# Performance work log

Measured on AMD Instinct MI355X. Metric: run time of the kernel, lower is better.

## Reference

```python
import jax, jax.numpy as jnp
import numpy as np

S = 4096          # seq_len (longformer-large-4096)
H = 1024          # hidden_size
FF = 3072         # ffnn_size (hardcoded)
G = 100           # number of gold mentions
MAX_SPAN = 30     # max_span_length
TOP_LAMBDA = 0.2
LN_EPS = 1e-5
MASK_VAL = 10000.0


def setup_inputs() -> dict:
    key = jax.random.key(0)
    ks = jax.random.split(key, 16)
    sc = 0.02
    sequence_output = jax.random.normal(ks[0], (1, S, H), jnp.float32)
    attention_mask = jnp.ones((1, S), jnp.int32)
    # valid gold spans: 1 <= start <= end < start + MAX_SPAN (so torch's >0 filter keeps all)
    gs = jax.random.randint(ks[1], (G,), 1, S - MAX_SPAN)
    gl = jax.random.randint(ks[2], (G,), 0, MAX_SPAN)
    gold_mentions = jnp.stack([gs, gs + gl], axis=1).astype(jnp.int32)  # [G, 2]
    inp = {
        'sequence_output': sequence_output,
        'attention_mask': attention_mask,
        'gold_mentions': gold_mentions,
        # start_mention_mlp
        'W_sm': jax.random.normal(ks[3], (H, FF), jnp.float32) * sc,
        'b_sm': jnp.zeros((FF,), jnp.float32),
        'g_sm': jnp.ones((FF,), jnp.float32),
        'beta_sm': jnp.zeros((FF,), jnp.float32),
        # end_mention_mlp
        'W_em': jax.random.normal(ks[4], (H, FF), jnp.float32) * sc,
        'b_em': jnp.zeros((FF,), jnp.float32),
        'g_em': jnp.ones((FF,), jnp.float32),
        'beta_em': jnp.zeros((FF,), jnp.float32),
        # classifiers
        'w_start': jax.random.normal(ks[5], (FF,), jnp.float32) * sc,
        'b_start': jnp.zeros((), jnp.float32),
        'w_end': jax.random.normal(ks[6], (FF,), jnp.float32) * sc,
        'b_end': jnp.zeros((), jnp.float32),
        'W_s2e': jax.random.normal(ks[7], (FF, FF), jnp.float32) * sc,
        'b_s2e': jnp.zeros((FF,), jnp.float32),
    }
    return inp


def _fcl(x, W, b, g, beta):
    # dense -> gelu (exact) -> layernorm (dropout is identity in eval)
    h = jax.nn.gelu(x @ W + b, approximate=False)
    mu = jnp.mean(h, axis=-1, keepdims=True)
    var = jnp.mean(jnp.square(h - mu), axis=-1, keepdims=True)
    return (h - mu) * jax.lax.rsqrt(var + LN_EPS) * g + beta


def _forward(sequence_output, attention_mask, gold_mentions,
             W_sm, b_sm, g_sm, beta_sm, W_em, b_em, g_em, beta_em,
             w_start, b_start, w_end, b_end, W_s2e, b_s2e):
    start_reps = _fcl(sequence_output, W_sm, b_sm, g_sm, beta_sm)  # [1,S,FF]
    end_reps = _fcl(sequence_output, W_em, b_em, g_em, beta_em)    # [1,S,FF]

    start_logits = jnp.einsum('bsf,f->bs', start_reps, w_start) + b_start  # [1,S]
    end_logits = jnp.einsum('bsf,f->bs', end_reps, w_end) + b_end          # [1,S]
    temp = start_reps @ W_s2e + b_s2e                                      # [1,S,FF]
    joint = jnp.einsum('bsf,btf->bst', temp, end_reps)                     # [1,S,S]
    mention_logits = joint + start_logits[:, :, None] + end_logits[:, None, :]

    # span mask: start <= end < start + MAX_SPAN (triu(0) then tril(MAX_SPAN-1))
    i = jnp.arange(S)
    mention_mask = ((i[:, None] <= i[None, :]) & (i[None, :] < i[:, None] + MAX_SPAN)
                    ).astype(jnp.float32)[None]  # [1,S,S]
    mention_logits = jnp.clip(mention_logits + (1.0 - mention_mask) * (-MASK_VAL),
                              -MASK_VAL, MASK_VAL)

    # top-k pruning; attention_mask is full so k is static: int(S * 0.2)
    max_k = int(S * TOP_LAMBDA)  # 819
    _, topk_1d = jax.lax.top_k(mention_logits.reshape(1, -1), max_k)  # [1,max_k]
    sorted_idx = jnp.sort(topk_1d, axis=-1)
    topk_start_ids = sorted_idx // S
    topk_end_ids = sorted_idx % S
    span_mask = jnp.ones((1, max_k), jnp.float32)

    # losses
    probs = jax.nn.sigmoid(mention_logits)  # [1,S,S]
    gstart = gold_mentions[:, 0]
    gend = gold_mentions[:, 1]
    gold_probs = probs[0, gstart, gend]
    # torch BCE clamps log at -100
    cost_gold = -jnp.mean(jnp.maximum(jnp.log(gold_probs), -100.0))
    junk = probs.at[0, gstart, gend].set(0.0)
    log1mp = jnp.maximum(jnp.log(1.0 - junk), -100.0)
    cost_junk = -jnp.sum(jnp.where(mention_mask == 1.0, log1mp, 0.0)) / jnp.sum(mention_mask)
    cost_is_mention = (cost_gold + cost_junk)[None]  # [1]

    return topk_start_ids, topk_end_ids, span_mask, sequence_output, cost_is_mention


def reference(sequence_output, attention_mask, gold_mentions,
              W_sm, b_sm, g_sm, beta_sm, W_em, b_em, g_em, beta_em,
              w_start, b_start, w_end, b_end, W_s2e, b_s2e):
    return _forward(sequence_output, attention_mask, gold_mentions,
                    W_sm, b_sm, g_sm, beta_sm, W_em, b_em, g_em, beta_em,
                    w_start, b_start, w_end, b_end, W_s2e, b_s2e)
```

## Files before the change

kernel.cpp:

```cpp
#include <hip/hip_runtime.h>
#include <math.h>

#define S 4096
#define H 1024
#define FF 3072
#define G 100
#define MAXSPAN 30
#define MAXK 819
#define NBAND (S * MAXSPAN)
#define BAND_COUNT 122445.0

#define O_START 0
#define O_END   819
#define O_MASK  1638
#define O_SEQ   2457
#define O_COST  (2457 + S * H)

typedef __bf16 bf16x8 __attribute__((ext_vector_type(8)));
typedef float f32x4 __attribute__((ext_vector_type(4)));
typedef float f32x16 __attribute__((ext_vector_type(16)));


__device__ __forceinline__ float block_reduce_256(float x, volatile float* red) {
  #pragma unroll
  for (int off = 32; off > 0; off >>= 1) x += __shfl_down(x, off, 64);
  int wid = threadIdx.x >> 6;
  int lane = threadIdx.x & 63;
  __syncthreads();
  if (lane == 0) red[wid] = x;
  __syncthreads();
  return red[0] + red[1] + red[2] + red[3];
}

__device__ __forceinline__ unsigned f2key(float f) {
  unsigned b = __float_as_uint(f);
  return (b & 0x80000000u) ? ~b : (b | 0x80000000u);
}

__device__ __forceinline__ unsigned short bf16_rne(float x) {
  unsigned u = __float_as_uint(x);
  unsigned r = ((u >> 16) & 1u) + 0x7FFFu;
  return (unsigned short)((u + r) >> 16);
}

__device__ __forceinline__ void split2(float x, unsigned short& h, unsigned short& l) {
  h = bf16_rne(x);
  float hf = __uint_as_float(((unsigned)h) << 16);
  l = bf16_rne(x - hf);
}

__device__ __forceinline__ void gld16(const void* g, void* l) {
  __builtin_amdgcn_global_load_lds(
      (const __attribute__((address_space(1))) unsigned int*)g,
      (__attribute__((address_space(3))) unsigned int*)l, 16, 0, 0);
}


__global__ __launch_bounds__(256) void pack_a_kernel(const float* __restrict__ A,
                                                     unsigned short* __restrict__ hi,
                                                     unsigned short* __restrict__ lo,
                                                     int K) {
  __shared__ float tile[32][33];
  const int t = threadIdx.x;
  const int tx = t & 31, ty8 = t >> 5;
  const int k0 = blockIdx.x * 32, r0 = blockIdx.y * 32;
  #pragma unroll
  for (int r = ty8; r < 32; r += 8)
    tile[r][tx] = A[(size_t)(r0 + r) * K + k0 + tx];
  __syncthreads();
  if (t < 128) {
    const int kql = t >> 5;
    const int rl = t & 31;
    unsigned short h8[8], l8[8];
    #pragma unroll
    for (int s = 0; s < 8; s++) split2(tile[rl][kql * 8 + s], h8[s], l8[s]);
    const size_t panel = (size_t)(r0 >> 7);
    const int rloc = (r0 & 127) + rl;
    const size_t off = panel * (size_t)(128 * K) + (size_t)(k0 / 8 + kql) * 1024 + (size_t)rloc * 8;
    *(uint4*)(hi + off) = *(const uint4*)h8;
    *(uint4*)(lo + off) = *(const uint4*)l8;
  }
}

__global__ __launch_bounds__(256) void pack_ln_a_kernel(const float* __restrict__ A,
                                                        const float* __restrict__ mu,
                                                        const float* __restrict__ rstd,
                                                        const float* __restrict__ g,
                                                        const float* __restrict__ beta,
                                                        unsigned short* __restrict__ hi,
                                                        unsigned short* __restrict__ lo,
                                                        int K) {
  __shared__ float tile[32][33];
  const int t = threadIdx.x;
  const int tx = t & 31, ty8 = t >> 5;
  const int k0 = blockIdx.x * 32, r0 = blockIdx.y * 32;
  #pragma unroll
  for (int r = ty8; r < 32; r += 8)
    tile[r][tx] = A[(size_t)(r0 + r) * K + k0 + tx];
  __syncthreads();
  if (t < 128) {
    const int kql = t >> 5;
    const int rl = t & 31;
    const int row = r0 + rl;
    const float m = mu[row], rs = rstd[row];
    float4 g0 = *(const float4*)(g + k0 + kql * 8);
    float4 g1 = *(const float4*)(g + k0 + kql * 8 + 4);
    float4 b0 = *(const float4*)(beta + k0 + kql * 8);
    float4 b1 = *(const float4*)(beta + k0 + kql * 8 + 4);
    float gv[8] = {g0.x, g0.y, g0.z, g0.w, g1.x, g1.y, g1.z, g1.w};
    float bv[8] = {b0.x, b0.y, b0.z, b0.w, b1.x, b1.y, b1.z, b1.w};
    unsigned short h8[8], l8[8];
    #pragma unroll
    for (int s = 0; s < 8; s++) {
      float v = (tile[rl][kql * 8 + s] - m) * rs * gv[s] + bv[s];
      split2(v, h8[s], l8[s]);
    }
    const size_t panel = (size_t)(r0 >> 7);
    const int rloc = (r0 & 127) + rl;
    const size_t off = panel * (size_t)(128 * K) + (size_t)(k0 / 8 + kql) * 1024 + (size_t)rloc * 8;
    *(uint4*)(hi + off) = *(const uint4*)h8;
    *(uint4*)(lo + off) = *(const uint4*)l8;
  }
}

__global__ __launch_bounds__(256) void pack_bt_kernel(const float* __restrict__ W,
                                                      unsigned short* __restrict__ hi,
                                                      unsigned short* __restrict__ lo,
                                                      int K, int N) {
  __shared__ float tile[32][33];
  const int t = threadIdx.x;
  const int tx = t & 31, ty8 = t >> 5;
  const int k0 = blockIdx.x * 32, n0 = blockIdx.y * 32;
  #pragma unroll
  for (int r = ty8; r < 32; r += 8)
    tile[r][tx] = W[(size_t)(k0 + r) * N + n0 + tx];
  __syncthreads();
  if (t < 128) {
    const int kql = t >> 5;
    const int nl = t & 31;
    unsigned short h8[8], l8[8];
    #pragma unroll
    for (int s = 0; s < 8; s++) split2(tile[kql * 8 + s][nl], h8[s], l8[s]);
    const size_t panel = (size_t)(n0 >> 7);
    const int nloc = (n0 & 127) + nl;
    const size_t off = panel * (size_t)(128 * K) + (size_t)(k0 / 8 + kql) * 1024 + (size_t)nloc * 8;
    *(uint4*)(hi + off) = *(const uint4*)h8;
    *(uint4*)(lo + off) = *(const uint4*)l8;
  }
}


template <int EPI>
__global__ __launch_bounds__(256) void gemm_mfma_kernel(const unsigned short* __restrict__ Ahi,
                                                        const unsigned short* __restrict__ Alo,
                                                        const unsigned short* __restrict__ Bhi,
                                                        const unsigned short* __restrict__ Blo,
                                                        const float* __restrict__ bias,
                                                        float* __restrict__ C,
                                                        int M, int N, int K) {
  __shared__ __align__(16) char smem[32768];
  const int tid = threadIdx.x;
  const int lane = tid & 63;
  const int wid = __builtin_amdgcn_readfirstlane(tid >> 6);
  const int wm = wid >> 1, wn = wid & 1;
  const int bm = blockIdx.y * 128, bn = blockIdx.x * 128;

  const size_t panAb = (size_t)blockIdx.y * (size_t)(128 * K) * 2;
  const size_t panBb = (size_t)blockIdx.x * (size_t)(128 * K) * 2;
  const char* cAh = (const char*)Ahi + panAb;
  const char* cAl = (const char*)Alo + panAb;
  const char* cBh = (const char*)Bhi + panBb;
  const char* cBl = (const char*)Blo + panBb;
  const int lb = lane * 16;
  const int ldsq = wid * 2048;

  const int khalf = lane >> 5;
  const int r31 = lane & 31;
  const int abase = khalf * 2048 + (wm * 64 + r31) * 16;
  const int bbase = khalf * 2048 + (wn * 64 + r31) * 16;

  f32x16 acc[2][2];
  #pragma unroll
  for (int a = 0; a < 2; a++)
    #pragma unroll
    for (int b = 0; b < 2; b++)
      #pragma unroll
      for (int r = 0; r < 16; r++) acc[a][b][r] = 0.0f;

  for (int k0 = 0; k0 < K; k0 += 32) {
    const size_t qb = (size_t)((k0 >> 3) + wid) * 2048 + lb;
    __syncthreads();
    gld16(cAh + qb,        smem +     0 + ldsq);
    gld16(cAh + qb + 1024, smem +     0 + ldsq + 1024);
    gld16(cAl + qb,        smem +  8192 + ldsq);
    gld16(cAl + qb + 1024, smem +  8192 + ldsq + 1024);
    gld16(cBh + qb,        smem + 16384 + ldsq);
    gld16(cBh + qb + 1024, smem + 16384 + ldsq + 1024);
    gld16(cBl + qb,        smem + 24576 + ldsq);
    gld16(cBl + qb + 1024, smem + 24576 + ldsq + 1024);
    __syncthreads();

    bf16x8 ah[2][2], al[2][2], bh[2][2], bl[2][2];
    #pragma unroll
    for (int ks = 0; ks < 2; ks++) {
      #pragma unroll
      for (int mt = 0; mt < 2; mt++) {
        ah[ks][mt] = *(const bf16x8*)(smem +     0 + ks * 4096 + abase + mt * 512);
        al[ks][mt] = *(const bf16x8*)(smem +  8192 + ks * 4096 + abase + mt * 512);
      }
      #pragma unroll
      for (int nt = 0; nt < 2; nt++) {
        bh[ks][nt] = *(const bf16x8*)(smem + 16384 + ks * 4096 + bbase + nt * 512);
        bl[ks][nt] = *(const bf16x8*)(smem + 24576 + ks * 4096 + bbase + nt * 512);
      }
    }
    #pragma unroll
    for (int ks = 0; ks < 2; ks++)
      #pragma unroll
      for (int mt = 0; mt < 2; mt++)
        #pragma unroll
        for (int nt = 0; nt < 2; nt++) {
          acc[mt][nt] = __builtin_amdgcn_mfma_f32_32x32x16_bf16(ah[ks][mt], bh[ks][nt], acc[mt][nt], 0, 0, 0);
          acc[mt][nt] = __builtin_amdgcn_mfma_f32_32x32x16_bf16(al[ks][mt], bh[ks][nt], acc[mt][nt], 0, 0, 0);
          acc[mt][nt] = __builtin_amdgcn_mfma_f32_32x32x16_bf16(ah[ks][mt], bl[ks][nt], acc[mt][nt], 0, 0, 0);
        }
  }

  #pragma unroll
  for (int mt = 0; mt < 2; mt++) {
    #pragma unroll
    for (int nt = 0; nt < 2; nt++) {
      const int colg = bn + wn * 64 + nt * 32 + r31;
      const float bb = bias[colg];
      #pragma unroll
      for (int reg = 0; reg < 16; reg++) {
        const int rowl = (reg & 3) + 8 * (reg >> 2) + 4 * khalf;
        const int rowg = bm + wm * 64 + mt * 32 + rowl;
        float v = acc[mt][nt][reg] + bb;
        if (EPI == 1) v = 0.5f * v * (1.0f + erff(v * 0.70710678118654752f));
        C[(size_t)rowg * N + colg] = v;
      }
    }
  }
}


template <int WRITEBACK>
__global__ __launch_bounds__(256) void ln_dot_kernel(float* __restrict__ Hb,
                                                     const float* __restrict__ g,
                                                     const float* __restrict__ beta,
                                                     const float* __restrict__ w,
                                                     const float* __restrict__ bsc,
                                                     float* __restrict__ logits,
                                                     float* __restrict__ mu_out,
                                                     float* __restrict__ rstd_out) {
  __shared__ float red[4];
  const int row = blockIdx.x, tid = threadIdx.x;
  float* h = Hb + (size_t)row * FF;

  float4 v[3];
  float s = 0.0f;
  #pragma unroll
  for (int t = 0; t < 3; t++) {
    v[t] = *(const float4*)(h + tid * 4 + t * 1024);
    s += v[t].x + v[t].y + v[t].z + v[t].w;
  }
  float mu = block_reduce_256(s, red) * (1.0f / (float)FF);

  float s2 = 0.0f;
  #pragma unroll
  for (int t = 0; t < 3; t++) {
    float dx = v[t].x - mu, dy = v[t].y - mu, dz = v[t].z - mu, dw = v[t].w - mu;
    s2 += dx * dx + dy * dy + dz * dz + dw * dw;
  }
  float var = block_reduce_256(s2, red) * (1.0f / (float)FF);
  float rstd = rsqrtf(var + 1e-5f);

  float dot = 0.0f;
  #pragma unroll
  for (int t = 0; t < 3; t++) {
    int idx = tid * 4 + t * 1024;
    float4 gv = *(const float4*)(g + idx);
    float4 bv = *(const float4*)(beta + idx);
    float4 wv = *(const float4*)(w + idx);
    float4 r;
    r.x = (v[t].x - mu) * rstd * gv.x + bv.x;
    r.y = (v[t].y - mu) * rstd * gv.y + bv.y;
    r.z = (v[t].z - mu) * rstd * gv.z + bv.z;
    r.w = (v[t].w - mu) * rstd * gv.w + bv.w;
    if (WRITEBACK) *(float4*)(h + idx) = r;
    dot += r.x * wv.x + r.y * wv.y + r.z * wv.z + r.w * wv.w;
  }
  float dt = block_reduce_256(dot, red);
  if (tid == 0) {
    logits[row] = dt + bsc[0];
    if (!WRITEBACK) { mu_out[row] = mu; rstd_out[row] = rstd; }
  }
}


__global__ __launch_bounds__(256) void band_joint_kernel(const float* __restrict__ T,
                                                         const float* __restrict__ E,
                                                         const float* __restrict__ sl,
                                                         const float* __restrict__ el,
                                                         float* __restrict__ band) {
  __shared__ float Elds[45][260];
  const int t = threadIdx.x;
  const int i0 = blockIdx.x * 16;
  const int r_l = t >> 4, c = t & 15;

  float accd[MAXSPAN];
  #pragma unroll
  for (int d = 0; d < MAXSPAN; d++) accd[d] = 0.0f;

  for (int k0 = 0; k0 < FF; k0 += 256) {
    const float* trow = T + (size_t)(i0 + r_l) * FF + k0 + c * 16;
    float4 tv0 = *(const float4*)(trow + 0);
    float4 tv1 = *(const float4*)(trow + 4);
    float4 tv2 = *(const float4*)(trow + 8);
    float4 tv3 = *(const float4*)(trow + 12);
    __syncthreads();
    for (int rr = t >> 6; rr < 45; rr += 4) {
      int gr = i0 + rr;
      int cc = (t & 63) * 4;
      float4 ev = {0.f, 0.f, 0.f, 0.f};
      if (gr < S) ev = *(const float4*)(E + (size_t)gr * FF + k0 + cc);
      *(float4*)&Elds[rr][cc] = ev;
    }
    __syncthreads();
    #pragma unroll
    for (int d = 0; d < MAXSPAN; d++) {
      const float* er = &Elds[r_l + d][c * 16];
      float4 e0 = *(const float4*)(er + 0);
      float4 e1 = *(const float4*)(er + 4);
      float4 e2 = *(const float4*)(er + 8);
      float4 e3 = *(const float4*)(er + 12);
      accd[d] += tv0.x * e0.x + tv0.y * e0.y + tv0.z * e0.z + tv0.w * e0.w
               + tv1.x * e1.x + tv1.y * e1.y + tv1.z * e1.z + tv1.w * e1.w
               + tv2.x * e2.x + tv2.y * e2.y + tv2.z * e2.z + tv2.w * e2.w
               + tv3.x * e3.x + tv3.y * e3.y + tv3.z * e3.z + tv3.w * e3.w;
    }
  }

  const int i = i0 + r_l;
  const float my_sl = sl[i];
  #pragma unroll
  for (int d = 0; d < MAXSPAN; d++) {
    float v = accd[d];
    v += __shfl_down(v, 8, 16);
    v += __shfl_down(v, 4, 16);
    v += __shfl_down(v, 2, 16);
    v += __shfl_down(v, 1, 16);
    if (c == 0) {
      int j = i + d;
      if (j < S) {
        float vv = v + my_sl + el[j];
        vv = fminf(fmaxf(vv, -10000.0f), 10000.0f);
        band[i * MAXSPAN + d] = vv;
      } else {
        band[i * MAXSPAN + d] = -1e30f;
      }
    }
  }
}


__global__ void mark_gold_kernel(const int* __restrict__ gold, char* __restrict__ mark) {
  int t = threadIdx.x;
  if (t < G) {
    int gs = gold[2 * t], ge = gold[2 * t + 1];
    mark[gs * MAXSPAN + (ge - gs)] = 1;
  }
}

__global__ __launch_bounds__(256) void cost_junk_kernel(const float* __restrict__ band,
                                                        const char* __restrict__ mark,
                                                        double* __restrict__ jacc) {
  __shared__ float red[4];
  int e = blockIdx.x * 256 + threadIdx.x;
  int i = e / MAXSPAN, d = e - i * MAXSPAN;
  float term = 0.0f;
  if (i + d < S && !mark[e]) {
    float x = band[e];
    float p = 1.0f / (1.0f + expf(-x));
    term = fmaxf(logf(1.0f - p), -100.0f);
  }
  float ssum = block_reduce_256(term, red);
  if (threadIdx.x == 0) atomicAdd(jacc, (double)ssum);
}

__global__ __launch_bounds__(256) void finalize_kernel(const float* __restrict__ band,
                                                       const int* __restrict__ gold,
                                                       const double* __restrict__ jacc,
                                                       float* __restrict__ outc) {
  __shared__ float red[4];
  int t = threadIdx.x;
  float term = 0.0f;
  if (t < G) {
    int gs = gold[2 * t], ge = gold[2 * t + 1];
    float x = band[gs * MAXSPAN + (ge - gs)];
    float p = 1.0f / (1.0f + expf(-x));
    term = fmaxf(logf(p), -100.0f);
  }
  float sg = block_reduce_256(term, red);
  if (t == 0) {
    double cost = -((double)sg / (double)G) - ((*jacc) / BAND_COUNT);
    *outc = (float)cost;
  }
}


__global__ __launch_bounds__(1024) void topk_kernel(const float* __restrict__ band,
                                                    float* __restrict__ out) {
  __shared__ int hist[256];
  __shared__ unsigned sh_prefix;
  __shared__ int sh_remk;
  __shared__ int idxbuf[1024];
  __shared__ int tiebuf[64];
  __shared__ int cnt_gt, cnt_eq;
  __shared__ int sb[1024];
  const int tid = threadIdx.x;

  unsigned prefix = 0;
  int remk = MAXK;
  for (int pass = 0; pass < 4; pass++) {
    int shift = 24 - pass * 8;
    if (tid < 256) hist[tid] = 0;
    __syncthreads();
    for (int e = tid; e < NBAND; e += 1024) {
      unsigned key = f2key(band[e]);
      bool match = (pass == 0) || ((key >> (shift + 8)) == prefix);
      if (match) atomicAdd(&hist[(key >> shift) & 255], 1);
    }
    __syncthreads();
    if (tid == 0) {
      int cum = 0, b = 255;
      for (; b > 0; b--) {
        if (cum + hist[b] >= remk) break;
        cum += hist[b];
      }
      sh_prefix = (prefix << 8) | (unsigned)b;
      sh_remk = remk - cum;
    }
    __syncthreads();
    prefix = sh_prefix;
    remk = sh_remk;
    __syncthreads();
  }
  const unsigned T = prefix;

  if (tid == 0) { cnt_gt = 0; cnt_eq = 0; }
  __syncthreads();
  for (int e = tid; e < NBAND; e += 1024) {
    unsigned key = f2key(band[e]);
    if (key >= T) {
      int i = e / MAXSPAN, d = e - i * MAXSPAN;
      int fi = i * S + i + d;
      if (key > T) {
        int p = atomicAdd(&cnt_gt, 1);
        if (p < 1024) idxbuf[p] = fi;
      } else {
        int p = atomicAdd(&cnt_eq, 1);
        if (p < 64) tiebuf[p] = fi;
      }
    }
  }
  __syncthreads();
  if (tid == 0) {
    int ngt = cnt_gt < 1024 ? cnt_gt : 1024;
    int ne = cnt_eq < 64 ? cnt_eq : 64;
    for (int a2 = 1; a2 < ne; a2++) {
      int kv = tiebuf[a2];
      int b2 = a2 - 1;
      while (b2 >= 0 && tiebuf[b2] > kv) { tiebuf[b2 + 1] = tiebuf[b2]; b2--; }
      tiebuf[b2 + 1] = kv;
    }
    int take = remk < ne ? remk : ne;
    for (int q = 0; q < take; q++)
      if (ngt + q < 1024) idxbuf[ngt + q] = tiebuf[q];
  }
  __syncthreads();

  sb[tid] = (tid < MAXK) ? idxbuf[tid] : 0x7FFFFFFF;
  __syncthreads();
  for (int ksz = 2; ksz <= 1024; ksz <<= 1) {
    for (int jj = ksz >> 1; jj > 0; jj >>= 1) {
      int ixj = tid ^ jj;
      if (ixj > tid) {
        int a2 = sb[tid], b2 = sb[ixj];
        bool up = ((tid & ksz) == 0);
        if (up ? (a2 > b2) : (a2 < b2)) { sb[tid] = b2; sb[ixj] = a2; }
      }
      __syncthreads();
    }
  }
  if (tid < MAXK) {
    int fi = sb[tid];
    out[O_START + tid] = (float)(fi >> 12);
    out[O_END + tid]   = (float)(fi & 4095);
    out[O_MASK + tid]  = 1.0f;
  }
}


extern "C" void kernel_launch(void* const* d_in, const int* in_sizes, int n_in,
                              void* d_out, int out_size, void* d_ws, size_t ws_size,
                              hipStream_t stream) {
  (void)in_sizes; (void)n_in; (void)out_size; (void)ws_size;
  const float* seq    = (const float*)d_in[0];
  const int*   gold   = (const int*)d_in[2];
  const float* W_sm   = (const float*)d_in[3];
  const float* b_sm   = (const float*)d_in[4];
  const float* g_sm   = (const float*)d_in[5];
  const float* be_sm  = (const float*)d_in[6];
  const float* W_em   = (const float*)d_in[7];
  const float* b_em   = (const float*)d_in[8];
  const float* g_em   = (const float*)d_in[9];
  const float* be_em  = (const float*)d_in[10];
  const float* w_st   = (const float*)d_in[11];
  const float* b_st   = (const float*)d_in[12];
  const float* w_en   = (const float*)d_in[13];
  const float* b_en   = (const float*)d_in[14];
  const float* W_s2e  = (const float*)d_in[15];
  const float* b_s2e  = (const float*)d_in[16];
  float* out = (float*)d_out;
  char* ws = (char*)d_ws;

  const size_t SZ_REP = (size_t)S * FF * 4;
  float*  bufS = (float*)(ws);
  float*  bufE = (float*)(ws + SZ_REP);
  float*  bufT = (float*)(ws + 2 * SZ_REP);
  char* R3 = ws + 3 * SZ_REP;
  unsigned short* seqhi = (unsigned short*)R3;
  unsigned short* seqlo = (unsigned short*)(R3 + (size_t)S * H * 2);
  unsigned short* a3hi  = (unsigned short*)R3;
  unsigned short* a3lo  = (unsigned short*)(R3 + (size_t)S * FF * 2);
  char* R4 = ws + 4 * SZ_REP;
  unsigned short* wbhi = (unsigned short*)R4;
  unsigned short* wblo = (unsigned short*)(R4 + (size_t)FF * FF * 2);
  char* R5 = R4 + 2 * (size_t)FF * FF * 2;
  float*  band = (float*)R5;
  char*   mark = R5 + (size_t)NBAND * 4;
  double* jacc = (double*)(R5 + (size_t)NBAND * 4 + NBAND + 32);
  float*  slog = (float*)(R5 + (size_t)NBAND * 4 + NBAND + 128);
  float*  elog = slog + S;
  float*  muS  = elog + S;
  float*  rstdS = muS + S;

  hipMemsetAsync(mark, 0, NBAND, stream);
  hipMemsetAsync(jacc, 0, 8, stream);

  dim3 gg(FF / 128, S / 128);

  pack_a_kernel<<<dim3(H / 32, S / 32), 256, 0, stream>>>(seq, seqhi, seqlo, H);
  pack_bt_kernel<<<dim3(H / 32, FF / 32), 256, 0, stream>>>(W_sm, wbhi, wblo, H, FF);
  gemm_mfma_kernel<1><<<gg, 256, 0, stream>>>(seqhi, seqlo, wbhi, wblo, b_sm, bufS, S, FF, H);
  ln_dot_kernel<0><<<S, 256, 0, stream>>>(bufS, g_sm, be_sm, w_st, b_st, slog, muS, rstdS);
  pack_bt_kernel<<<dim3(H / 32, FF / 32), 256, 0, stream>>>(W_em, wbhi, wblo, H, FF);
  gemm_mfma_kernel<1><<<gg, 256, 0, stream>>>(seqhi, seqlo, wbhi, wblo, b_em, bufE, S, FF, H);
  ln_dot_kernel<1><<<S, 256, 0, stream>>>(bufE, g_em, be_em, w_en, b_en, elog, nullptr, nullptr);
  pack_ln_a_kernel<<<dim3(FF / 32, S / 32), 256, 0, stream>>>(bufS, muS, rstdS, g_sm, be_sm, a3hi, a3lo, FF);
  pack_bt_kernel<<<dim3(FF / 32, FF / 32), 256, 0, stream>>>(W_s2e, wbhi, wblo, FF, FF);
  gemm_mfma_kernel<0><<<gg, 256, 0, stream>>>(a3hi, a3lo, wbhi, wblo, b_s2e, bufT, S, FF, FF);

  band_joint_kernel<<<S / 16, 256, 0, stream>>>(bufT, bufE, slog, elog, band);

  mark_gold_kernel<<<1, 128, 0, stream>>>(gold, mark);
  cost_junk_kernel<<<NBAND / 256, 256, 0, stream>>>(band, mark, jacc);
  topk_kernel<<<1, 1024, 0, stream>>>(band, out);
  finalize_kernel<<<1, 256, 0, stream>>>(band, gold, jacc, out + O_COST);

  hipMemcpyAsync(out + O_SEQ, seq, (size_t)S * H * 4, hipMemcpyDeviceToDevice, stream);
}
```

Measured before the change: 839.4 us.

## Batch start/end GEMMs, merge LN stats, fold end-LN into band kernel, shorten top-k radix

The two first-layer GEMMs now run as one launch with a z dimension, and the two layernorm/dot kernels become one stats-only kernel. The end-MLP layernorm writeback is dropped; band_joint_kernel applies the normalization on the fly when staging E into LDS, and its block order is swizzled. The top-k radix select stops after two 8-bit passes instead of four, and ties are resolved with a larger key+index insertion sort. This trades fewer launches and less memory traffic for extra ALU work in the band kernel and a possibly long serial tie sort on one thread.

```diff
diff --git a/kernel.cpp b/kernel.cpp
--- a/kernel.cpp
+++ b/kernel.cpp
@@ -151,26 +151,16 @@
 
 
 template <int EPI>
-__global__ __launch_bounds__(256) void gemm_mfma_kernel(const unsigned short* __restrict__ Ahi,
-                                                        const unsigned short* __restrict__ Alo,
-                                                        const unsigned short* __restrict__ Bhi,
-                                                        const unsigned short* __restrict__ Blo,
-                                                        const float* __restrict__ bias,
-                                                        float* __restrict__ C,
-                                                        int M, int N, int K) {
-  __shared__ __align__(16) char smem[32768];
+__device__ __forceinline__ void gemm_body(const char* cAh, const char* cAl,
+                                          const char* cBh, const char* cBl,
+                                          const float* __restrict__ bias,
+                                          float* __restrict__ C,
+                                          int bm, int bn, int N, int K,
+                                          char* smem) {
   const int tid = threadIdx.x;
   const int lane = tid & 63;
   const int wid = __builtin_amdgcn_readfirstlane(tid >> 6);
   const int wm = wid >> 1, wn = wid & 1;
-  const int bm = blockIdx.y * 128, bn = blockIdx.x * 128;
-
-  const size_t panAb = (size_t)blockIdx.y * (size_t)(128 * K) * 2;
-  const size_t panBb = (size_t)blockIdx.x * (size_t)(128 * K) * 2;
-  const char* cAh = (const char*)Ahi + panAb;
-  const char* cAl = (const char*)Alo + panAb;
-  const char* cBh = (const char*)Bhi + panBb;
-  const char* cBl = (const char*)Blo + panBb;
   const int lb = lane * 16;
   const int ldsq = wid * 2048;
 
@@ -244,19 +234,71 @@
   }
 }
 
-
-template <int WRITEBACK>
-__global__ __launch_bounds__(256) void ln_dot_kernel(float* __restrict__ Hb,
-                                                     const float* __restrict__ g,
-                                                     const float* __restrict__ beta,
-                                                     const float* __restrict__ w,
-                                                     const float* __restrict__ bsc,
-                                                     float* __restrict__ logits,
-                                                     float* __restrict__ mu_out,
-                                                     float* __restrict__ rstd_out) {
+__global__ __launch_bounds__(256) void gemm_mfma_kernel(const unsigned short* __restrict__ Ahi,
+                                                        const unsigned short* __restrict__ Alo,
+                                                        const unsigned short* __restrict__ Bhi,
+                                                        const unsigned short* __restrict__ Blo,
+                                                        const float* __restrict__ bias,
+                                                        float* __restrict__ C,
+                                                        int N, int K) {
+  __shared__ __align__(16) char smem[32768];
+  const size_t panAb = (size_t)blockIdx.y * (size_t)(128 * K) * 2;
+  const size_t panBb = (size_t)blockIdx.x * (size_t)(128 * K) * 2;
+  gemm_body<0>((const char*)Ahi + panAb, (const char*)Alo + panAb,
+               (const char*)Bhi + panBb, (const char*)Blo + panBb,
+               bias, C, blockIdx.y * 128, blockIdx.x * 128, N, K, smem);
+}
+
+__global__ __launch_bounds__(256) void gemm_mfma_dual_kernel(const unsigned short* __restrict__ Ahi,
+                                                             const unsigned short* __restrict__ Alo,
+                                                             const unsigned short* __restrict__ B1hi,
+                                                             const unsigned short* __restrict__ B1lo,
+                                                             const unsigned short* __restrict__ B2hi,
+                                                             const unsigned short* __restrict__ B2lo,
+                                                             const float* __restrict__ bias1,
+                                                             const float* __restrict__ bias2,
+                                                             float* __restrict__ C1,
+                                                             float* __restrict__ C2,
+                                                             int N, int K) {
+  __shared__ __align__(16) char smem[32768];
+  const int zb = blockIdx.z;
+  const unsigned short* Bhi = zb ? B2hi : B1hi;
+  const unsigned short* Blo = zb ? B2lo : B1lo;
+  const float* bias = zb ? bias2 : bias1;
+  float* C = zb ? C2 : C1;
+  const size_t panAb = (size_t)blockIdx.y * (size_t)(128 * K) * 2;
+  const size_t panBb = (size_t)blockIdx.x * (size_t)(128 * K) * 2;
+  gemm_body<1>((const char*)Ahi + panAb, (const char*)Alo + panAb,
+               (const char*)Bhi + panBb, (const char*)Blo + panBb,
+               bias, C, blockIdx.y * 128, blockIdx.x * 128, N, K, smem);
+}
+
+
+__global__ __launch_bounds__(256) void ln_stats_kernel(const float* __restrict__ HbS,
+                                                       const float* __restrict__ HbE,
+                                                       const float* __restrict__ gS,
+                                                       const float* __restrict__ betaS,
+                                                       const float* __restrict__ wS,
+                                                       const float* __restrict__ bS,
+                                                       const float* __restrict__ gE,
+                                                       const float* __restrict__ betaE,
+                                                       const float* __restrict__ wE,
+                                                       const float* __restrict__ bE,
+                                                       float* __restrict__ slog,
+                                                       float* __restrict__ elog,
+                                                       float* __restrict__ muS,
+                                                       float* __restrict__ rstdS,
+                                                       float* __restrict__ muE,
+                                                       float* __restrict__ rstdE) {
   __shared__ float red[4];
   const int row = blockIdx.x, tid = threadIdx.x;
-  float* h = Hb + (size_t)row * FF;
+  const int br = blockIdx.y;
+  const float* Hb = br ? HbE : HbS;
+  const float* g = br ? gE : gS;
+  const float* beta = br ? betaE : betaS;
+  const float* w = br ? wE : wS;
+  const float* bsc = br ? bE : bS;
+  const float* h = Hb + (size_t)row * FF;
 
   float4 v[3];
   float s = 0.0f;
@@ -283,30 +325,34 @@
     float4 gv = *(const float4*)(g + idx);
     float4 bv = *(const float4*)(beta + idx);
     float4 wv = *(const float4*)(w + idx);
-    float4 r;
-    r.x = (v[t].x - mu) * rstd * gv.x + bv.x;
-    r.y = (v[t].y - mu) * rstd * gv.y + bv.y;
-    r.z = (v[t].z - mu) * rstd * gv.z + bv.z;
-    r.w = (v[t].w - mu) * rstd * gv.w + bv.w;
-    if (WRITEBACK) *(float4*)(h + idx) = r;
-    dot += r.x * wv.x + r.y * wv.y + r.z * wv.z + r.w * wv.w;
+    float rx = (v[t].x - mu) * rstd * gv.x + bv.x;
+    float ry = (v[t].y - mu) * rstd * gv.y + bv.y;
+    float rz = (v[t].z - mu) * rstd * gv.z + bv.z;
+    float rw = (v[t].w - mu) * rstd * gv.w + bv.w;
+    dot += rx * wv.x + ry * wv.y + rz * wv.z + rw * wv.w;
   }
   float dt = block_reduce_256(dot, red);
   if (tid == 0) {
-    logits[row] = dt + bsc[0];
-    if (!WRITEBACK) { mu_out[row] = mu; rstd_out[row] = rstd; }
+    if (br) { elog[row] = dt + bsc[0]; muE[row] = mu; rstdE[row] = rstd; }
+    else    { slog[row] = dt + bsc[0]; muS[row] = mu; rstdS[row] = rstd; }
   }
 }
 
 
 __global__ __launch_bounds__(256) void band_joint_kernel(const float* __restrict__ T,
-                                                         const float* __restrict__ E,
+                                                         const float* __restrict__ Eraw,
+                                                         const float* __restrict__ muE,
+                                                         const float* __restrict__ rstdE,
+                                                         const float* __restrict__ gE,
+                                                         const float* __restrict__ betaE,
                                                          const float* __restrict__ sl,
                                                          const float* __restrict__ el,
                                                          float* __restrict__ band) {
   __shared__ float Elds[45][260];
   const int t = threadIdx.x;
-  const int i0 = blockIdx.x * 16;
+  const int bx = blockIdx.x;
+  const int sbx = (bx & 7) * 32 + (bx >> 3);
+  const int i0 = sbx * 16;
   const int r_l = t >> 4, c = t & 15;
 
   float accd[MAXSPAN];
@@ -323,9 +369,18 @@
     for (int rr = t >> 6; rr < 45; rr += 4) {
       int gr = i0 + rr;
       int cc = (t & 63) * 4;
-      float4 ev = {0.f, 0.f, 0.f, 0.f};
-      if (gr < S) ev = *(const float4*)(E + (size_t)gr * FF + k0 + cc);
-      *(float4*)&Elds[rr][cc] = ev;
+      float4 rv = {0.f, 0.f, 0.f, 0.f};
+      if (gr < S) {
+        float4 ev = *(const float4*)(Eraw + (size_t)gr * FF + k0 + cc);
+        float m = muE[gr], rs = rstdE[gr];
+        float4 gv = *(const float4*)(gE + k0 + cc);
+        float4 bv = *(const float4*)(betaE + k0 + cc);
+        rv.x = (ev.x - m) * rs * gv.x + bv.x;
+        rv.y = (ev.y - m) * rs * gv.y + bv.y;
+        rv.z = (ev.z - m) * rs * gv.z + bv.z;
+        rv.w = (ev.w - m) * rs * gv.w + bv.w;
+      }
+      *(float4*)&Elds[rr][cc] = rv;
     }
     __syncthreads();
     #pragma unroll
@@ -416,68 +471,83 @@
   __shared__ unsigned sh_prefix;
   __shared__ int sh_remk;
   __shared__ int idxbuf[1024];
-  __shared__ int tiebuf[64];
+  __shared__ unsigned tkey[256];
+  __shared__ int tidx[256];
   __shared__ int cnt_gt, cnt_eq;
   __shared__ int sb[1024];
   const int tid = threadIdx.x;
 
-  unsigned prefix = 0;
-  int remk = MAXK;
-  for (int pass = 0; pass < 4; pass++) {
-    int shift = 24 - pass * 8;
-    if (tid < 256) hist[tid] = 0;
-    __syncthreads();
-    for (int e = tid; e < NBAND; e += 1024) {
-      unsigned key = f2key(band[e]);
-      bool match = (pass == 0) || ((key >> (shift + 8)) == prefix);
-      if (match) atomicAdd(&hist[(key >> shift) & 255], 1);
-    }
-    __syncthreads();
-    if (tid == 0) {
-      int cum = 0, b = 255;
-      for (; b > 0; b--) {
-        if (cum + hist[b] >= remk) break;
-        cum += hist[b];
-      }
-      sh_prefix = (prefix << 8) | (unsigned)b;
-      sh_remk = remk - cum;
-    }
-    __syncthreads();
-    prefix = sh_prefix;
-    remk = sh_remk;
-    __syncthreads();
-  }
-  const unsigned T = prefix;
-
-  if (tid == 0) { cnt_gt = 0; cnt_eq = 0; }
+  if (tid < 256) hist[tid] = 0;
+  __syncthreads();
+  for (int e = tid; e < NBAND; e += 1024)
+    atomicAdd(&hist[f2key(band[e]) >> 24], 1);
+  __syncthreads();
+  if (tid == 0) {
+    int cum = 0, b = 255;
+    for (; b > 0; b--) {
+      if (cum + hist[b] >= MAXK) break;
+      cum += hist[b];
+    }
+    sh_prefix = (unsigned)b;
+    sh_remk = MAXK - cum;
+  }
+  __syncthreads();
+  const unsigned p8 = sh_prefix;
+  int remk = sh_remk;
+  __syncthreads();
+
+  if (tid < 256) hist[tid] = 0;
   __syncthreads();
   for (int e = tid; e < NBAND; e += 1024) {
     unsigned key = f2key(band[e]);
-    if (key >= T) {
+    if ((key >> 24) == p8) atomicAdd(&hist[(key >> 16) & 255], 1);
+  }
+  __syncthreads();
+  if (tid == 0) {
+    int cum = 0, b = 255;
+    for (; b > 0; b--) {
+      if (cum + hist[b] >= remk) break;
+      cum += hist[b];
+    }
+    sh_prefix = (p8 << 8) | (unsigned)b;
+    sh_remk = remk - cum;
+  }
+  __syncthreads();
+  const unsigned T16 = sh_prefix;
+  remk = sh_remk;
+
+  if (tid == 0) { cnt_gt = 0; cnt_eq = 0; }
+  __syncthreads();
+  for (int e = tid; e < NBAND; e += 1024) {
+    unsigned key = f2key(band[e]);
+    unsigned k16 = key >> 16;
+    if (k16 >= T16) {
       int i = e / MAXSPAN, d = e - i * MAXSPAN;
       int fi = i * S + i + d;
-      if (key > T) {
+      if (k16 > T16) {
         int p = atomicAdd(&cnt_gt, 1);
         if (p < 1024) idxbuf[p] = fi;
       } else {
         int p = atomicAdd(&cnt_eq, 1);
-        if (p < 64) tiebuf[p] = fi;
+        if (p < 256) { tkey[p] = key; tidx[p] = fi; }
       }
     }
   }
   __syncthreads();
   if (tid == 0) {
     int ngt = cnt_gt < 1024 ? cnt_gt : 1024;
-    int ne = cnt_eq < 64 ? cnt_eq : 64;
+    int ne = cnt_eq < 256 ? cnt_eq : 256;
     for (int a2 = 1; a2 < ne; a2++) {
-      int kv = tiebuf[a2];
+      unsigned kv = tkey[a2]; int iv = tidx[a2];
       int b2 = a2 - 1;
-      while (b2 >= 0 && tiebuf[b2] > kv) { tiebuf[b2 + 1] = tiebuf[b2]; b2--; }
-      tiebuf[b2 + 1] = kv;
+      while (b2 >= 0 && (tkey[b2] < kv || (tkey[b2] == kv && tidx[b2] > iv))) {
+        tkey[b2 + 1] = tkey[b2]; tidx[b2 + 1] = tidx[b2]; b2--;
+      }
+      tkey[b2 + 1] = kv; tidx[b2 + 1] = iv;
     }
     int take = remk < ne ? remk : ne;
     for (int q = 0; q < take; q++)
-      if (ngt + q < 1024) idxbuf[ngt + q] = tiebuf[q];
+      if (ngt + q < 1024) idxbuf[ngt + q] = tidx[q];
   }
   __syncthreads();
 
@@ -536,6 +606,11 @@
   unsigned short* a3hi  = (unsigned short*)R3;
   unsigned short* a3lo  = (unsigned short*)(R3 + (size_t)S * FF * 2);
   char* R4 = ws + 4 * SZ_REP;
+  const size_t SZ_W12 = (size_t)H * FF * 2;
+  unsigned short* wb1hi = (unsigned short*)R4;
+  unsigned short* wb1lo = (unsigned short*)(R4 + SZ_W12);
+  unsigned short* wb2hi = (unsigned short*)(R4 + 2 * SZ_W12);
+  unsigned short* wb2lo = (unsigned short*)(R4 + 3 * SZ_W12);
   unsigned short* wbhi = (unsigned short*)R4;
   unsigned short* wblo = (unsigned short*)(R4 + (size_t)FF * FF * 2);
   char* R5 = R4 + 2 * (size_t)FF * FF * 2;
@@ -543,27 +618,32 @@
   char*   mark = R5 + (size_t)NBAND * 4;
   double* jacc = (double*)(R5 + (size_t)NBAND * 4 + NBAND + 32);
   float*  slog = (float*)(R5 + (size_t)NBAND * 4 + NBAND + 128);
-  float*  elog = slog + S;
-  float*  muS  = elog + S;
+  float*  elog  = slog + S;
+  float*  muS   = elog + S;
   float*  rstdS = muS + S;
+  float*  muE   = rstdS + S;
+  float*  rstdE = muE + S;
 
   hipMemsetAsync(mark, 0, NBAND, stream);
   hipMemsetAsync(jacc, 0, 8, stream);
 
   dim3 gg(FF / 128, S / 128);
+  dim3 gg2(FF / 128, S / 128, 2);
 
   pack_a_kernel<<<dim3(H / 32, S / 32), 256, 0, stream>>>(seq, seqhi, seqlo, H);
-  pack_bt_kernel<<<dim3(H / 32, FF / 32), 256, 0, stream>>>(W_sm, wbhi, wblo, H, FF);
-  gemm_mfma_kernel<1><<<gg, 256, 0, stream>>>(seqhi, seqlo, wbhi, wblo, b_sm, bufS, S, FF, H);
-  ln_dot_kernel<0><<<S, 256, 0, stream>>>(bufS, g_sm, be_sm, w_st, b_st, slog, muS, rstdS);
-  pack_bt_kernel<<<dim3(H / 32, FF / 32), 256, 0, stream>>>(W_em, wbhi, wblo, H, FF);
-  gemm_mfma_kernel<1><<<gg, 256, 0, stream>>>(seqhi, seqlo, wbhi, wblo, b_em, bufE, S, FF, H);
-  ln_dot_kernel<1><<<S, 256, 0, stream>>>(bufE, g_em, be_em, w_en, b_en, elog, nullptr, nullptr);
+  pack_bt_kernel<<<dim3(H / 32, FF / 32), 256, 0, stream>>>(W_sm, wb1hi, wb1lo, H, FF);
+  pack_bt_kernel<<<dim3(H / 32, FF / 32), 256, 0, stream>>>(W_em, wb2hi, wb2lo, H, FF);
+  gemm_mfma_dual_kernel<<<gg2, 256, 0, stream>>>(seqhi, seqlo, wb1hi, wb1lo, wb2hi, wb2lo,
+                                                 b_sm, b_em, bufS, bufE, FF, H);
+  ln_stats_kernel<<<dim3(S, 2), 256, 0, stream>>>(bufS, bufE, g_sm, be_sm, w_st, b_st,
+                                                  g_em, be_em, w_en, b_en,
+                                                  slog, elog, muS, rstdS, muE, rstdE);
   pack_ln_a_kernel<<<dim3(FF / 32, S / 32), 256, 0, stream>>>(bufS, muS, rstdS, g_sm, be_sm, a3hi, a3lo, FF);
   pack_bt_kernel<<<dim3(FF / 32, FF / 32), 256, 0, stream>>>(W_s2e, wbhi, wblo, FF, FF);
-  gemm_mfma_kernel<0><<<gg, 256, 0, stream>>>(a3hi, a3lo, wbhi, wblo, b_s2e, bufT, S, FF, FF);
-
-  band_joint_kernel<<<S / 16, 256, 0, stream>>>(bufT, bufE, slog, elog, band);
+  gemm_mfma_kernel<<<gg, 256, 0, stream>>>(a3hi, a3lo, wbhi, wblo, b_s2e, bufT, FF, FF);
+
+  band_joint_kernel<<<S / 16, 256, 0, stream>>>(bufT, bufE, muE, rstdE, g_em, be_em,
+                                                slog, elog, band);
 
   mark_gold_kernel<<<1, 128, 0, stream>>>(gold, mark);
   cost_junk_kernel<<<NBAND / 256, 256, 0, stream>>>(band, mark, jacc);
```

New measurement: 824.3 us. Within noise of the previous version (-1.8%).
